# Kernel tuning notes

Measured on AMD Instinct MI355X. Metric: run time of the kernel, lower is better.

The kernel has to match this reference:

```python
import jax, jax.numpy as jnp
import numpy as np

HIDDEN = 768
NUM_HEADS = 12
HEAD_DIM = HIDDEN // NUM_HEADS


def setup_inputs() -> dict:
    key = jax.random.key(0)
    ks = jax.random.split(key, 10)
    B, S = 4, 2048
    scale = 1.0 / np.sqrt(HIDDEN)
    inp = {
        "hidden_states": jax.random.normal(ks[0], (B, S, HIDDEN), dtype=jnp.float32),
        "attention_mask": jnp.ones((B, S), dtype=jnp.float32),
        "Wq": jax.random.normal(ks[1], (HIDDEN, HIDDEN), dtype=jnp.float32) * scale,
        "bq": jnp.zeros((HIDDEN,), dtype=jnp.float32),
        "Wk": jax.random.normal(ks[2], (HIDDEN, HIDDEN), dtype=jnp.float32) * scale,
        "bk": jnp.zeros((HIDDEN,), dtype=jnp.float32),
        "Wv": jax.random.normal(ks[3], (HIDDEN, HIDDEN), dtype=jnp.float32) * scale,
        "bv": jnp.zeros((HIDDEN,), dtype=jnp.float32),
        "Wo": jax.random.normal(ks[4], (HIDDEN, HIDDEN), dtype=jnp.float32) * scale,
        "bo": jnp.zeros((HIDDEN,), dtype=jnp.float32),
    }
    return inp


def _split_heads(x):
    # [B,S,H] -> [B,nh,S,dh]
    B, S, _ = x.shape
    return x.reshape(B, S, NUM_HEADS, HEAD_DIM).transpose(0, 2, 1, 3)


def reference(hidden_states, attention_mask, Wq, bq, Wk, bk, Wv, bv, Wo, bo):
    # Linear projections (torch nn.Linear: x @ W.T + b; here W stored as [in,out])
    q = _split_heads(hidden_states @ Wq + bq)
    k = _split_heads(hidden_states @ Wk + bk)
    v = _split_heads(hidden_states @ Wv + bv)

    # scores: [B,nh,S,S]
    scores = jnp.einsum("bhqd,bhkd->bhqk", q, k) / np.sqrt(HEAD_DIM).astype(np.float32)

    # outer-product mask: [B,1,S,S], broadcast over heads
    ext = (attention_mask[:, :, None] * attention_mask[:, None, :])[:, None, :, :]
    scores = ext * scores - (1.0 - ext) * 1e9

    probs = jax.nn.softmax(scores, axis=-1)
    ctx = jnp.einsum("bhqk,bhkd->bhqd", probs, v)  # [B,nh,S,dh]
    B, _, S, _ = ctx.shape
    ctx = ctx.transpose(0, 2, 1, 3).reshape(B, S, HIDDEN)
    out = ctx @ Wo + bo
    # torch F.gelu default: exact (erf-based)
    return jax.nn.gelu(out, approximate=False)
```

## Files before the change

### kernel.cpp

```cpp
#include <hip/hip_runtime.h>
#include <math.h>

#define HIDDEN 768
#define NH 12
#define DH 64
#define SEQ 2048
#define BATCH 4

typedef __bf16 bf16;
typedef bf16 bf16x4 __attribute__((ext_vector_type(4)));
typedef bf16 bf16x8 __attribute__((ext_vector_type(8)));
typedef float f32x4 __attribute__((ext_vector_type(4)));

__global__ __launch_bounds__(256) void prep_x(const float* __restrict__ X,
                                              bf16* __restrict__ Xb) {
    const size_t i = ((size_t)blockIdx.x * 256 + threadIdx.x) * 8;
    float4 a = *(const float4*)(X + i);
    float4 b = *(const float4*)(X + i + 4);
    bf16x8 o = {(bf16)a.x, (bf16)a.y, (bf16)a.z, (bf16)a.w,
                (bf16)b.x, (bf16)b.y, (bf16)b.z, (bf16)b.w};
    *(bf16x8*)(Xb + i) = o;
}

__global__ __launch_bounds__(256) void prep_w(const float* __restrict__ Wq,
                                              const float* __restrict__ Wk,
                                              const float* __restrict__ Wv,
                                              const float* __restrict__ Wo,
                                              bf16* __restrict__ Wt,
                                              bf16* __restrict__ Wot_hi,
                                              bf16* __restrict__ Wot_lo) {
    __shared__ float Ts[64][68];
    const int tid = threadIdx.x;
    const int n0 = blockIdx.x * 64, k0 = blockIdx.y * 64, z = blockIdx.z;
    const float* W = (z == 0) ? Wq : (z == 1) ? Wk : (z == 2) ? Wv : Wo;

    {
        const int r = tid >> 2, c = (tid & 3) << 4;
        const float* src = W + (size_t)(k0 + r) * HIDDEN + n0 + c;
#pragma unroll
        for (int j = 0; j < 4; ++j)
            *(float4*)&Ts[r][c + 4 * j] = *(const float4*)(src + 4 * j);
    }
    __syncthreads();

    const int nl = tid >> 2, kc = (tid & 3) << 4;
    float v[16];
#pragma unroll
    for (int j = 0; j < 16; ++j) v[j] = Ts[kc + j][nl];

    if (z < 3) {
        bf16 hi[16];
#pragma unroll
        for (int j = 0; j < 16; ++j) hi[j] = (bf16)v[j];
        const size_t off = (size_t)(z * HIDDEN + n0 + nl) * HIDDEN + k0 + kc;
        *(bf16x8*)(Wt + off) = *(bf16x8*)&hi[0];
        *(bf16x8*)(Wt + off + 8) = *(bf16x8*)&hi[8];
    } else {
        bf16 hi[16], lo[16];
#pragma unroll
        for (int j = 0; j < 16; ++j) {
            hi[j] = (bf16)v[j];
            lo[j] = (bf16)(v[j] - (float)hi[j]);
        }
        const size_t off = (size_t)(n0 + nl) * HIDDEN + k0 + kc;
        *(bf16x8*)(Wot_hi + off) = *(bf16x8*)&hi[0];
        *(bf16x8*)(Wot_hi + off + 8) = *(bf16x8*)&hi[8];
        *(bf16x8*)(Wot_lo + off) = *(bf16x8*)&lo[0];
        *(bf16x8*)(Wot_lo + off + 8) = *(bf16x8*)&lo[8];
    }
}

__global__ __launch_bounds__(256) void gemm_qkv(
    const bf16* __restrict__ Xb, const bf16* __restrict__ Wt,
    const float* __restrict__ bq, const float* __restrict__ bk,
    const float* __restrict__ bv, bf16* __restrict__ q_out,
    bf16* __restrict__ k_out, bf16* __restrict__ v_out) {
    __shared__ bf16 As[128][40];
    __shared__ bf16 Bs[128][40];

    const int tid = threadIdx.x;
    const int ln = tid & 63, wv = tid >> 6;
    const int quad = ln >> 4, l16 = ln & 15;
    const int wm = wv >> 1, wn = wv & 1;
    const int n0 = blockIdx.x * 128, m0 = blockIdx.y * 128;

    f32x4 acc[4][4];
#pragma unroll
    for (int i = 0; i < 4; ++i)
#pragma unroll
        for (int j = 0; j < 4; ++j) acc[i][j] = (f32x4){0.f, 0.f, 0.f, 0.f};

    const int sr = tid >> 1, sc = (tid & 1) << 4;
    const bf16* gA = Xb + (size_t)(m0 + sr) * HIDDEN + sc;
    const bf16* gB = Wt + (size_t)(n0 + sr) * HIDDEN + sc;

    bf16x8 ar0, ar1, br0, br1;
    ar0 = *(const bf16x8*)gA;
    ar1 = *(const bf16x8*)(gA + 8);
    br0 = *(const bf16x8*)gB;
    br1 = *(const bf16x8*)(gB + 8);

    for (int k0 = 0; k0 < HIDDEN; k0 += 32) {
        __syncthreads();
        *(bf16x8*)&As[sr][sc] = ar0;
        *(bf16x8*)&As[sr][sc + 8] = ar1;
        *(bf16x8*)&Bs[sr][sc] = br0;
        *(bf16x8*)&Bs[sr][sc + 8] = br1;
        __syncthreads();
        if (k0 + 32 < HIDDEN) {
            ar0 = *(const bf16x8*)(gA + k0 + 32);
            ar1 = *(const bf16x8*)(gA + k0 + 40);
            br0 = *(const bf16x8*)(gB + k0 + 32);
            br1 = *(const bf16x8*)(gB + k0 + 40);
        }

        bf16x8 ah[4], bh[4];
#pragma unroll
        for (int i = 0; i < 4; ++i) {
            ah[i] = *(bf16x8*)&As[wm * 64 + i * 16 + l16][quad * 8];
            bh[i] = *(bf16x8*)&Bs[wn * 64 + i * 16 + l16][quad * 8];
        }
#pragma unroll
        for (int mi = 0; mi < 4; ++mi)
#pragma unroll
            for (int ni = 0; ni < 4; ++ni)
                acc[mi][ni] = __builtin_amdgcn_mfma_f32_16x16x32_bf16(
                    ah[mi], bh[ni], acc[mi][ni], 0, 0, 0);
    }

    const int nb = n0 + wn * 64;
    const int which = nb / HIDDEN;
    const int nrel = nb - which * HIDDEN;
    const int h = nrel >> 6;

    if (which < 2) {
        const float scale = (which == 0) ? 0.125f : 1.0f;
        const float* bias = (which == 0) ? bq : bk;
        bf16* dst = (which == 0) ? q_out : k_out;
#pragma unroll
        for (int ni = 0; ni < 4; ++ni) {
            const int dh = ni * 16 + l16;
            const float bb = bias[nrel + dh];
#pragma unroll
            for (int mi = 0; mi < 4; ++mi)
#pragma unroll
                for (int r = 0; r < 4; ++r) {
                    const int m = m0 + wm * 64 + mi * 16 + quad * 4 + r;
                    const int bi = m >> 11, s = m & (SEQ - 1);
                    dst[(((size_t)(bi * NH + h) * SEQ + s) << 6) + dh] =
                        (bf16)(scale * (acc[mi][ni][r] + bb));
                }
        }
    } else {
        const int bi = m0 >> 11;
        const int sbase = (m0 & (SEQ - 1)) + wm * 64;
#pragma unroll
        for (int ni = 0; ni < 4; ++ni) {
            const int dh = ni * 16 + l16;
            const float bb = bv[nrel + dh];
            bf16* vrow = v_out + ((size_t)(bi * NH + h) * DH + dh) * SEQ;
#pragma unroll
            for (int mi = 0; mi < 4; ++mi) {
                bf16x4 pk = {(bf16)(acc[mi][ni][0] + bb),
                             (bf16)(acc[mi][ni][1] + bb),
                             (bf16)(acc[mi][ni][2] + bb),
                             (bf16)(acc[mi][ni][3] + bb)};
                *(bf16x4*)(vrow + sbase + mi * 16 + quad * 4) = pk;
            }
        }
    }
}

__global__ __launch_bounds__(256) void attn_mfma(const bf16* __restrict__ Q,
                                                 const bf16* __restrict__ K,
                                                 const bf16* __restrict__ Vt,
                                                 const float* __restrict__ mask,
                                                 float* __restrict__ ctx) {
    __shared__ bf16 Ks[64][72];
    __shared__ bf16 Vts[64][72];
    __shared__ bf16 Ps[128][72];
    __shared__ float Ms[SEQ];
    __shared__ int allones_s;

    const int tid = threadIdx.x;
    const int ln = tid & 63, w = tid >> 6;
    const int quad = ln >> 4, l16 = ln & 15;
    const int qt = blockIdx.x, h = blockIdx.y, b = blockIdx.z;
    const size_t bh = (size_t)b * NH + h;
    const bf16* Qp = Q + ((bh * SEQ + (size_t)qt * 128) << 6);
    const bf16* Kp = K + (bh * SEQ << 6);
    const bf16* Vp = Vt + (bh * DH) * SEQ;

    if (tid == 0) allones_s = 1;
    {
        float4 m0 = *(const float4*)(mask + (size_t)b * SEQ + tid * 8);
        float4 m1 = *(const float4*)(mask + (size_t)b * SEQ + tid * 8 + 4);
        *(float4*)&Ms[tid * 8] = m0;
        *(float4*)&Ms[tid * 8 + 4] = m1;
        bool ok = (m0.x == 1.f) & (m0.y == 1.f) & (m0.z == 1.f) &
                  (m0.w == 1.f) & (m1.x == 1.f) & (m1.y == 1.f) &
                  (m1.z == 1.f) & (m1.w == 1.f);
        __syncthreads();
        if (!ok) allones_s = 0;
    }
    __syncthreads();
    const bool fastmask = (allones_s != 0);

    bf16x8 qb[2][2];
#pragma unroll
    for (int qg = 0; qg < 2; ++qg)
#pragma unroll
        for (int hf = 0; hf < 2; ++hf)
            qb[qg][hf] = *(const bf16x8*)(Qp + ((w * 32 + qg * 16 + l16) << 6) +
                                          hf * 32 + quad * 8);
    float mq[2];
#pragma unroll
    for (int qg = 0; qg < 2; ++qg)
        mq[qg] = Ms[qt * 128 + w * 32 + qg * 16 + l16];

    float l_i[2] = {0.f, 0.f};
    f32x4 acc[4][2];
#pragma unroll
    for (int fd = 0; fd < 4; ++fd)
#pragma unroll
        for (int qg = 0; qg < 2; ++qg) acc[fd][qg] = (f32x4){0.f, 0.f, 0.f, 0.f};

    const int sr = tid >> 2, sc = (tid & 3) << 4;
    const bf16* kbase = Kp + ((size_t)sr << 6) + sc;
    const bf16* vbase = Vp + (size_t)sr * SEQ + sc;

    bf16x8 kr0, kr1, vr0, vr1;
    kr0 = *(const bf16x8*)kbase;
    kr1 = *(const bf16x8*)(kbase + 8);
    vr0 = *(const bf16x8*)vbase;
    vr1 = *(const bf16x8*)(vbase + 8);

    for (int kt = 0; kt < SEQ / 64; ++kt) {
        __syncthreads();
        *(bf16x8*)&Ks[sr][sc] = kr0;
        *(bf16x8*)&Ks[sr][sc + 8] = kr1;
        *(bf16x8*)&Vts[sr][sc] = vr0;
        *(bf16x8*)&Vts[sr][sc + 8] = vr1;
        __syncthreads();
        if (kt + 1 < SEQ / 64) {
            kr0 = *(const bf16x8*)(kbase + ((size_t)(kt + 1) << 12));
            kr1 = *(const bf16x8*)(kbase + ((size_t)(kt + 1) << 12) + 8);
            vr0 = *(const bf16x8*)(vbase + (kt + 1) * 64);
            vr1 = *(const bf16x8*)(vbase + (kt + 1) * 64 + 8);
        }

        f32x4 st[4][2];
#pragma unroll
        for (int f = 0; f < 4; ++f) {
            bf16x8 ka0 = *(bf16x8*)&Ks[f * 16 + l16][quad * 8];
            bf16x8 ka1 = *(bf16x8*)&Ks[f * 16 + l16][32 + quad * 8];
#pragma unroll
            for (int qg = 0; qg < 2; ++qg) {
                f32x4 c = {0.f, 0.f, 0.f, 0.f};
                c = __builtin_amdgcn_mfma_f32_16x16x32_bf16(ka0, qb[qg][0], c, 0, 0, 0);
                c = __builtin_amdgcn_mfma_f32_16x16x32_bf16(ka1, qb[qg][1], c, 0, 0, 0);
                st[f][qg] = c;
            }
        }

        if (!fastmask) {
#pragma unroll
            for (int f = 0; f < 4; ++f) {
                const float4 mk4 = *(const float4*)&Ms[kt * 64 + f * 16 + quad * 4];
                const float mkk[4] = {mk4.x, mk4.y, mk4.z, mk4.w};
#pragma unroll
                for (int qg = 0; qg < 2; ++qg)
#pragma unroll
                    for (int r = 0; r < 4; ++r) {
                        const float ext = mq[qg] * mkk[r];
                        st[f][qg][r] = ext * st[f][qg][r] - (1.0f - ext) * 1e9f;
                    }
            }
        }

#pragma unroll
        for (int qg = 0; qg < 2; ++qg) {
#pragma unroll
            for (int f = 0; f < 4; ++f) {
                float p0 = __expf(st[f][qg][0]);
                float p1 = __expf(st[f][qg][1]);
                float p2 = __expf(st[f][qg][2]);
                float p3 = __expf(st[f][qg][3]);
                l_i[qg] += (p0 + p1) + (p2 + p3);
                bf16x4 pk = {(bf16)p0, (bf16)p1, (bf16)p2, (bf16)p3};
                *(bf16x4*)&Ps[w * 32 + qg * 16 + l16][f * 16 + quad * 4] = pk;
            }
        }

        bf16x8 pb[2][2];
#pragma unroll
        for (int qg = 0; qg < 2; ++qg)
#pragma unroll
            for (int hf = 0; hf < 2; ++hf)
                pb[qg][hf] =
                    *(bf16x8*)&Ps[w * 32 + qg * 16 + l16][hf * 32 + quad * 8];
#pragma unroll
        for (int fd = 0; fd < 4; ++fd) {
            bf16x8 va0 = *(bf16x8*)&Vts[fd * 16 + l16][quad * 8];
            bf16x8 va1 = *(bf16x8*)&Vts[fd * 16 + l16][32 + quad * 8];
#pragma unroll
            for (int qg = 0; qg < 2; ++qg) {
                f32x4 c = acc[fd][qg];
                c = __builtin_amdgcn_mfma_f32_16x16x32_bf16(va0, pb[qg][0], c, 0, 0, 0);
                c = __builtin_amdgcn_mfma_f32_16x16x32_bf16(va1, pb[qg][1], c, 0, 0, 0);
                acc[fd][qg] = c;
            }
        }
    }

#pragma unroll
    for (int qg = 0; qg < 2; ++qg) {
        l_i[qg] += __shfl_xor(l_i[qg], 16);
        l_i[qg] += __shfl_xor(l_i[qg], 32);
    }

#pragma unroll
    for (int qg = 0; qg < 2; ++qg) {
        const float inv = 1.0f / l_i[qg];
        const size_t row = (size_t)b * SEQ + qt * 128 + w * 32 + qg * 16 + l16;
#pragma unroll
        for (int fd = 0; fd < 4; ++fd) {
            float4 o = {acc[fd][qg][0] * inv, acc[fd][qg][1] * inv,
                        acc[fd][qg][2] * inv, acc[fd][qg][3] * inv};
            *(float4*)(ctx + row * HIDDEN + h * 64 + fd * 16 + quad * 4) = o;
        }
    }
}

__global__ __launch_bounds__(256) void gemm_out(const float* __restrict__ ctx,
                                                const bf16* __restrict__ Bhi,
                                                const bf16* __restrict__ Blo,
                                                const float* __restrict__ bo,
                                                float* __restrict__ fout) {
    __shared__ bf16 As_hi[128][40];
    __shared__ bf16 As_lo[128][40];
    __shared__ bf16 Bs_hi[64][40];
    __shared__ bf16 Bs_lo[64][40];

    const int tid = threadIdx.x;
    const int ln = tid & 63, wv = tid >> 6;
    const int quad = ln >> 4, l16 = ln & 15;
    const int wm = wv >> 1, wn = wv & 1;
    const int n0 = blockIdx.x * 64, m0 = blockIdx.y * 128;

    f32x4 acc[4][2];
#pragma unroll
    for (int i = 0; i < 4; ++i)
#pragma unroll
        for (int j = 0; j < 2; ++j) acc[i][j] = (f32x4){0.f, 0.f, 0.f, 0.f};

    const int sra = tid >> 1, sca = (tid & 1) << 4;
    const int srb = tid >> 2, scb = (tid & 3) << 3;
    const float* gA = ctx + (size_t)(m0 + sra) * HIDDEN + sca;
    const bf16* gBh = Bhi + (size_t)(n0 + srb) * HIDDEN + scb;
    const bf16* gBl = Blo + (size_t)(n0 + srb) * HIDDEN + scb;

    float fa[16];
    bf16x8 brh, brl;
#pragma unroll
    for (int j = 0; j < 4; ++j) *(float4*)&fa[4 * j] = *(const float4*)(gA + 4 * j);
    brh = *(const bf16x8*)gBh;
    brl = *(const bf16x8*)gBl;

    for (int k0 = 0; k0 < HIDDEN; k0 += 32) {
        bf16 hi[16], lo[16];
#pragma unroll
        for (int j = 0; j < 16; ++j) {
            hi[j] = (bf16)fa[j];
            lo[j] = (bf16)(fa[j] - (float)hi[j]);
        }
        __syncthreads();
        *(bf16x8*)&As_hi[sra][sca] = *(bf16x8*)&hi[0];
        *(bf16x8*)&As_hi[sra][sca + 8] = *(bf16x8*)&hi[8];
        *(bf16x8*)&As_lo[sra][sca] = *(bf16x8*)&lo[0];
        *(bf16x8*)&As_lo[sra][sca + 8] = *(bf16x8*)&lo[8];
        *(bf16x8*)&Bs_hi[srb][scb] = brh;
        *(bf16x8*)&Bs_lo[srb][scb] = brl;
        __syncthreads();
        if (k0 + 32 < HIDDEN) {
#pragma unroll
            for (int j = 0; j < 4; ++j)
                *(float4*)&fa[4 * j] = *(const float4*)(gA + k0 + 32 + 4 * j);
            brh = *(const bf16x8*)(gBh + k0 + 32);
            brl = *(const bf16x8*)(gBl + k0 + 32);
        }

        bf16x8 ah[4], al[4], bh[2], bl[2];
#pragma unroll
        for (int i = 0; i < 4; ++i) {
            ah[i] = *(bf16x8*)&As_hi[wm * 64 + i * 16 + l16][quad * 8];
            al[i] = *(bf16x8*)&As_lo[wm * 64 + i * 16 + l16][quad * 8];
        }
#pragma unroll
        for (int i = 0; i < 2; ++i) {
            bh[i] = *(bf16x8*)&Bs_hi[wn * 32 + i * 16 + l16][quad * 8];
            bl[i] = *(bf16x8*)&Bs_lo[wn * 32 + i * 16 + l16][quad * 8];
        }
#pragma unroll
        for (int mi = 0; mi < 4; ++mi)
#pragma unroll
            for (int ni = 0; ni < 2; ++ni) {
                f32x4 c = acc[mi][ni];
                c = __builtin_amdgcn_mfma_f32_16x16x32_bf16(ah[mi], bh[ni], c, 0, 0, 0);
                c = __builtin_amdgcn_mfma_f32_16x16x32_bf16(ah[mi], bl[ni], c, 0, 0, 0);
                c = __builtin_amdgcn_mfma_f32_16x16x32_bf16(al[mi], bh[ni], c, 0, 0, 0);
                acc[mi][ni] = c;
            }
    }

#pragma unroll
    for (int ni = 0; ni < 2; ++ni) {
        const int n = n0 + wn * 32 + ni * 16 + l16;
        const float bb = bo[n];
#pragma unroll
        for (int mi = 0; mi < 4; ++mi)
#pragma unroll
            for (int r = 0; r < 4; ++r) {
                const int m = m0 + wm * 64 + mi * 16 + quad * 4 + r;
                float x = acc[mi][ni][r] + bb;
                x = 0.5f * x * (1.0f + erff(x * 0.70710678118654752440f));
                fout[(size_t)m * HIDDEN + n] = x;
            }
    }
}

extern "C" void kernel_launch(void* const* d_in, const int* in_sizes, int n_in,
                              void* d_out, int out_size, void* d_ws, size_t ws_size,
                              hipStream_t stream) {
    const float* X    = (const float*)d_in[0];
    const float* mask = (const float*)d_in[1];
    const float* Wq   = (const float*)d_in[2];
    const float* bq   = (const float*)d_in[3];
    const float* Wk   = (const float*)d_in[4];
    const float* bk   = (const float*)d_in[5];
    const float* Wv   = (const float*)d_in[6];
    const float* bv   = (const float*)d_in[7];
    const float* Wo   = (const float*)d_in[8];
    const float* bo   = (const float*)d_in[9];
    float* out = (float*)d_out;

    char* w = (char*)d_ws;
    const size_t NE = (size_t)BATCH * SEQ * HIDDEN;
    bf16* q_ws   = (bf16*)w;  w += NE * 2;
    bf16* k_ws   = (bf16*)w;  w += NE * 2;
    bf16* vt_ws  = (bf16*)w;  w += NE * 2;
    float* ctx   = (float*)w; w += NE * 4;
    bf16* Xb     = (bf16*)w;  w += NE * 2;
    bf16* Wt     = (bf16*)w;  w += (size_t)3 * HIDDEN * HIDDEN * 2;
    bf16* Wot_hi = (bf16*)w;  w += (size_t)HIDDEN * HIDDEN * 2;
    bf16* Wot_lo = (bf16*)w;  w += (size_t)HIDDEN * HIDDEN * 2;

    prep_x<<<(int)(NE / 2048), 256, 0, stream>>>(X, Xb);
    prep_w<<<dim3(12, 12, 4), 256, 0, stream>>>(Wq, Wk, Wv, Wo, Wt, Wot_hi,
                                                Wot_lo);
    gemm_qkv<<<dim3(18, 64), 256, 0, stream>>>(Xb, Wt, bq, bk, bv, q_ws, k_ws,
                                               vt_ws);
    attn_mfma<<<dim3(SEQ / 128, NH, BATCH), 256, 0, stream>>>(q_ws, k_ws, vt_ws,
                                                              mask, ctx);
    gemm_out<<<dim3(12, 64), 256, 0, stream>>>(ctx, Wot_hi, Wot_lo, bo, out);
}
```

Measured before the change: 279.5 us.

## Load K/V fragments directly from global, drop LDS staging and barriers, use exp2

Removes the shared-memory staging of K and V tiles and both per-iteration __syncthreads. Each wave now reads its MFMA operands straight from global memory, relying on L1/L2 since all four waves read the same tiles. The P buffer becomes a flat XOR-swizzled array, dropping the padding. Softmax uses the hardware exp2, with log2(e) folded into the Q scale and the mask constant, which removes a multiply per element. The risk is that uncoalesced 16-byte global loads and four-fold redundant cache traffic stall the MFMAs without explicit prefetch.

```diff
diff --git a/kernel.cpp b/kernel.cpp
--- a/kernel.cpp
+++ b/kernel.cpp
@@ -134,7 +134,7 @@
     const int h = nrel >> 6;
 
     if (which < 2) {
-        const float scale = (which == 0) ? 0.125f : 1.0f;
+        const float scale = (which == 0) ? 0.18033688011112042f : 1.0f;
         const float* bias = (which == 0) ? bq : bk;
         bf16* dst = (which == 0) ? q_out : k_out;
 #pragma unroll
@@ -176,9 +176,7 @@
                                                  const bf16* __restrict__ Vt,
                                                  const float* __restrict__ mask,
                                                  float* __restrict__ ctx) {
-    __shared__ bf16 Ks[64][72];
-    __shared__ bf16 Vts[64][72];
-    __shared__ bf16 Ps[128][72];
+    __shared__ bf16 Ps[128 * 64];
     __shared__ float Ms[SEQ];
     __shared__ int allones_s;
 
@@ -225,35 +223,17 @@
 #pragma unroll
         for (int qg = 0; qg < 2; ++qg) acc[fd][qg] = (f32x4){0.f, 0.f, 0.f, 0.f};
 
-    const int sr = tid >> 2, sc = (tid & 3) << 4;
-    const bf16* kbase = Kp + ((size_t)sr << 6) + sc;
-    const bf16* vbase = Vp + (size_t)sr * SEQ + sc;
-
-    bf16x8 kr0, kr1, vr0, vr1;
-    kr0 = *(const bf16x8*)kbase;
-    kr1 = *(const bf16x8*)(kbase + 8);
-    vr0 = *(const bf16x8*)vbase;
-    vr1 = *(const bf16x8*)(vbase + 8);
-
+#pragma unroll 2
     for (int kt = 0; kt < SEQ / 64; ++kt) {
-        __syncthreads();
-        *(bf16x8*)&Ks[sr][sc] = kr0;
-        *(bf16x8*)&Ks[sr][sc + 8] = kr1;
-        *(bf16x8*)&Vts[sr][sc] = vr0;
-        *(bf16x8*)&Vts[sr][sc + 8] = vr1;
-        __syncthreads();
-        if (kt + 1 < SEQ / 64) {
-            kr0 = *(const bf16x8*)(kbase + ((size_t)(kt + 1) << 12));
-            kr1 = *(const bf16x8*)(kbase + ((size_t)(kt + 1) << 12) + 8);
-            vr0 = *(const bf16x8*)(vbase + (kt + 1) * 64);
-            vr1 = *(const bf16x8*)(vbase + (kt + 1) * 64 + 8);
-        }
+        const bf16* kp = Kp + ((size_t)kt << 12);
+        const bf16* vp = Vp + kt * 64;
 
         f32x4 st[4][2];
 #pragma unroll
         for (int f = 0; f < 4; ++f) {
-            bf16x8 ka0 = *(bf16x8*)&Ks[f * 16 + l16][quad * 8];
-            bf16x8 ka1 = *(bf16x8*)&Ks[f * 16 + l16][32 + quad * 8];
+            const bf16* krow = kp + ((f * 16 + l16) << 6) + quad * 8;
+            bf16x8 ka0 = *(const bf16x8*)krow;
+            bf16x8 ka1 = *(const bf16x8*)(krow + 32);
 #pragma unroll
             for (int qg = 0; qg < 2; ++qg) {
                 f32x4 c = {0.f, 0.f, 0.f, 0.f};
@@ -273,36 +253,44 @@
 #pragma unroll
                     for (int r = 0; r < 4; ++r) {
                         const float ext = mq[qg] * mkk[r];
-                        st[f][qg][r] = ext * st[f][qg][r] - (1.0f - ext) * 1e9f;
+                        st[f][qg][r] =
+                            ext * st[f][qg][r] - (1.0f - ext) * 1.4426950e9f;
                     }
             }
         }
 
 #pragma unroll
         for (int qg = 0; qg < 2; ++qg) {
+            const int row = w * 32 + qg * 16 + l16;
+            const int sw = (row & 7) << 3;
+            bf16* prow = &Ps[row * 64];
 #pragma unroll
             for (int f = 0; f < 4; ++f) {
-                float p0 = __expf(st[f][qg][0]);
-                float p1 = __expf(st[f][qg][1]);
-                float p2 = __expf(st[f][qg][2]);
-                float p3 = __expf(st[f][qg][3]);
+                float p0 = __builtin_amdgcn_exp2f(st[f][qg][0]);
+                float p1 = __builtin_amdgcn_exp2f(st[f][qg][1]);
+                float p2 = __builtin_amdgcn_exp2f(st[f][qg][2]);
+                float p3 = __builtin_amdgcn_exp2f(st[f][qg][3]);
                 l_i[qg] += (p0 + p1) + (p2 + p3);
                 bf16x4 pk = {(bf16)p0, (bf16)p1, (bf16)p2, (bf16)p3};
-                *(bf16x4*)&Ps[w * 32 + qg * 16 + l16][f * 16 + quad * 4] = pk;
+                *(bf16x4*)&prow[(f * 16 + quad * 4) ^ sw] = pk;
             }
         }
 
         bf16x8 pb[2][2];
 #pragma unroll
-        for (int qg = 0; qg < 2; ++qg)
+        for (int qg = 0; qg < 2; ++qg) {
+            const int row = w * 32 + qg * 16 + l16;
+            const int sw = (row & 7) << 3;
 #pragma unroll
             for (int hf = 0; hf < 2; ++hf)
                 pb[qg][hf] =
-                    *(bf16x8*)&Ps[w * 32 + qg * 16 + l16][hf * 32 + quad * 8];
+                    *(bf16x8*)&Ps[row * 64 + ((hf * 32 + quad * 8) ^ sw)];
+        }
 #pragma unroll
         for (int fd = 0; fd < 4; ++fd) {
-            bf16x8 va0 = *(bf16x8*)&Vts[fd * 16 + l16][quad * 8];
-            bf16x8 va1 = *(bf16x8*)&Vts[fd * 16 + l16][32 + quad * 8];
+            const bf16* vrow = vp + (size_t)(fd * 16 + l16) * SEQ + quad * 8;
+            bf16x8 va0 = *(const bf16x8*)vrow;
+            bf16x8 va1 = *(const bf16x8*)(vrow + 32);
 #pragma unroll
             for (int qg = 0; qg < 2; ++qg) {
                 f32x4 c = acc[fd][qg];
```

Result: slower. 430.4 us (+54.0%).
